# Kernel tuning notes

Hardware: AMD Instinct MI355X
Metric: run time of the kernel (lower is better)

Reference implementation:

```python
import jax, jax.numpy as jnp
import numpy as np

B, C, D, O = 64, 64, 512, 256
N_REG, G = 8, 8  # 8 regions of 8 channels


def setup_inputs() -> dict:
    key = jax.random.key(0)
    ks = jax.random.split(key, 9)
    std = 0.02  # init_weights_classify: normal(0, 0.02) for Linear weights, zero bias
    x = jax.random.normal(ks[0], (B, C, D), dtype=jnp.float32)
    region_indices = jnp.arange(C, dtype=jnp.int32).reshape(N_REG, G)
    # attn_fc: Linear(2D -> D), ReLU, Linear(D -> 1)
    W1 = jax.random.normal(ks[1], (2 * D, D), dtype=jnp.float32) * std
    b1 = jnp.zeros((D,), jnp.float32)
    W2 = jax.random.normal(ks[2], (D, 1), dtype=jnp.float32) * std
    b2 = jnp.zeros((1,), jnp.float32)
    # gcn1: Linear(D -> D); gcn2: Linear(D -> O)
    Wg1 = jax.random.normal(ks[3], (D, D), dtype=jnp.float32) * std
    bg1 = jnp.zeros((D,), jnp.float32)
    Wg2 = jax.random.normal(ks[4], (D, O), dtype=jnp.float32) * std
    bg2 = jnp.zeros((O,), jnp.float32)
    return {"x": x, "W1": W1, "b1": b1, "W2": W2, "b2": b2,
            "Wg1": Wg1, "bg1": bg1, "Wg2": Wg2, "bg2": bg2,
            "region_indices": region_indices}


def _leaky_relu02(z):
    return jnp.where(z >= 0, z, 0.2 * z)


def reference(x, W1, b1, W2, b2, Wg1, bg1, Wg2, bg2, region_indices):
    Bb, Cc, Dd = x.shape
    n_reg, g = region_indices.shape
    # channel -> region id; mask[i,j] = same region and i != j
    rid = jnp.zeros((Cc,), jnp.int32).at[region_indices.reshape(-1)].set(
        jnp.repeat(jnp.arange(n_reg, dtype=jnp.int32), g))
    idx = jnp.arange(Cc)
    mask = (rid[:, None] == rid[None, :]) & (idx[:, None] != idx[None, :])  # [C, C]
    # attn_fc on cat(x_i, x_j): split first linear to avoid [B,C,C,2D] concat
    a = x @ W1[:Dd]   # [B, C, D]
    bpart = x @ W1[Dd:]  # [B, C, D]
    h = jax.nn.relu(a[:, :, None, :] + bpart[:, None, :, :] + b1)  # [B, C, C, D]
    scores = jnp.einsum('bijd,do->bij', h, W2) + b2[0]  # [B, C, C]
    scores = jnp.where(mask[None, :, :], scores, -jnp.inf)
    adj = jax.nn.softmax(scores, axis=-1)  # [B, C, C]
    # gcn1: adj @ x -> Linear -> LeakyReLU(0.2); residual mix
    m1 = jnp.einsum('bij,bjd->bid', adj, x)
    x1 = _leaky_relu02(m1 @ Wg1 + bg1)
    x1 = 0.5 * x1 + 0.5 * x
    # gcn2
    m2 = jnp.einsum('bij,bjd->bid', adj, x1)
    out = _leaky_relu02(m2 @ Wg2 + bg2)  # [B, C, O]
    return out
```

## Files before the change

### kernel.cpp

```cpp
#include <hip/hip_runtime.h>
#include <math.h>

#define B_   64
#define C_   64
#define D_   512
#define O_   256
#define G_   8
#define M_   4096

typedef __attribute__((ext_vector_type(8))) short s16x8;
typedef __attribute__((ext_vector_type(4))) float f32x4;
typedef unsigned short u16;
typedef unsigned int   u32;

__device__ __forceinline__ float bf2f(u16 u) { return __uint_as_float(((u32)u) << 16); }
__device__ __forceinline__ u16 f2bf(float f) {
    u32 u = __float_as_uint(f);
    return (u16)((u + 0x7FFFu + ((u >> 16) & 1u)) >> 16);
}
__device__ __forceinline__ void gload16(const void* g, void* l) {
    __builtin_amdgcn_global_load_lds((const __attribute__((address_space(1))) u32*)g,
                                     (__attribute__((address_space(3))) u32*)l, 16, 0, 0);
}
__device__ __forceinline__ void xcd_swz(int& bx, int& by) {
    int nx = (int)gridDim.x;
    int L = bx + by * nx;
    int nwg = nx * (int)gridDim.y;
    int nid = (L & 7) * (nwg >> 3) + (L >> 3);
    bx = nid & (nx - 1);
    by = nid / nx;
}

__global__ __launch_bounds__(256)
void prep_kernel(const float* __restrict__ x, u16* __restrict__ x_bf,
                 const float* __restrict__ W1, u16* __restrict__ W1t,
                 const float* __restrict__ Wg1, u16* __restrict__ Wg1t,
                 const float* __restrict__ Wg2, u16* __restrict__ Wg2t)
{
    __shared__ float tile[32][33];
    const int bx = blockIdx.x, tid = threadIdx.x;
    if (bx < 1024) {
        size_t i = ((size_t)bx * 256 + tid) * 8;
        const float4* p = (const float4*)(x + i);
        float4 v0 = p[0], v1 = p[1];
        s16x8 o;
        o[0] = (short)f2bf(v0.x); o[1] = (short)f2bf(v0.y);
        o[2] = (short)f2bf(v0.z); o[3] = (short)f2bf(v0.w);
        o[4] = (short)f2bf(v1.x); o[5] = (short)f2bf(v1.y);
        o[6] = (short)f2bf(v1.z); o[7] = (short)f2bf(v1.w);
        *(s16x8*)(x_bf + i) = o;
        return;
    }
    const float* src; u16* dst; int k0, n0, nsrc, obase;
    if (bx < 1536) {
        int idx = bx - 1024, h = idx >> 8, t = idx & 255;
        src = W1 + (size_t)h * 512 * 512; dst = W1t; obase = h * 512;
        k0 = (t >> 4) * 32; n0 = (t & 15) * 32; nsrc = 512;
    } else if (bx < 1792) {
        int t = bx - 1536;
        src = Wg1; dst = Wg1t; obase = 0;
        k0 = (t >> 4) * 32; n0 = (t & 15) * 32; nsrc = 512;
    } else {
        int t = bx - 1792;
        src = Wg2; dst = Wg2t; obase = 0;
        k0 = (t >> 3) * 32; n0 = (t & 7) * 32; nsrc = 256;
    }
    int tx = tid & 31, ty = tid >> 5;
    #pragma unroll
    for (int j = 0; j < 4; j++)
        tile[ty + j * 8][tx] = src[(size_t)(k0 + ty + j * 8) * nsrc + n0 + tx];
    __syncthreads();
    #pragma unroll
    for (int j = 0; j < 4; j++)
        dst[(size_t)(obase + n0 + ty + j * 8) * 512 + k0 + tx] = f2bf(tile[tx][ty + j * 8]);
}

template<int BM, int BN, int EPI>
__global__ __launch_bounds__(256)
void mfma_gemm(const u16* __restrict__ A, const u16* __restrict__ Bt,
               u16* __restrict__ Obf0, u16* __restrict__ Obf1,
               const float* __restrict__ bias, float* __restrict__ Of)
{
    constexpr int K = 512, BK = 64, NT = K / BK;
    constexpr int MR = BM / 32, NR = BN / 32;
    constexpr int CA = BM / 32, CB = BN / 32;

    __shared__ __align__(16) u16 As[2][BM * BK];
    __shared__ __align__(16) u16 Bs[2][BN * BK];

    const int tid = threadIdx.x;
    const int lane = tid & 63;
    const int w = tid >> 6, wr = w >> 1, wc = w & 1;
    const int lr = lane & 15, lq = lane >> 4;
    int bx = blockIdx.x, by = blockIdx.y;
    xcd_swz(bx, by);
    const int m0 = by * BM, n0 = bx * BN;

    const int sr  = tid >> 3;
    const int ss  = tid & 7;
    const int gsl = ss ^ (sr & 7);

    f32x4 acc[MR][NR] = {};

    auto stage = [&](int buf, int kt) {
        #pragma unroll
        for (int ch = 0; ch < CA; ch++)
            gload16(A + (size_t)(m0 + ch * 32 + sr) * K + kt + gsl * 8,
                    &As[buf][ch * 2048 + tid * 8]);
        #pragma unroll
        for (int ch = 0; ch < CB; ch++)
            gload16(Bt + (size_t)(n0 + ch * 32 + sr) * K + kt + gsl * 8,
                    &Bs[buf][ch * 2048 + tid * 8]);
    };

    stage(0, 0);
    int cur = 0;
    for (int t = 0; t < NT; t++) {
        __syncthreads();
        if (t + 1 < NT) stage(cur ^ 1, (t + 1) * BK);
        const u16* as = As[cur]; const u16* bs = Bs[cur];
        #pragma unroll
        for (int ks = 0; ks < 2; ks++) {
            s16x8 af[MR], bfv[NR];
            #pragma unroll
            for (int m = 0; m < MR; m++) {
                int r = wr * (BM / 2) + m * 16 + lr;
                af[m] = *(const s16x8*)(as + r * 64 + (((ks * 4 + lq) ^ (r & 7)) * 8));
            }
            #pragma unroll
            for (int n = 0; n < NR; n++) {
                int r = wc * (BN / 2) + n * 16 + lr;
                bfv[n] = *(const s16x8*)(bs + r * 64 + (((ks * 4 + lq) ^ (r & 7)) * 8));
            }
            #pragma unroll
            for (int m = 0; m < MR; m++)
                #pragma unroll
                for (int n = 0; n < NR; n++)
                    acc[m][n] = __builtin_amdgcn_mfma_f32_16x16x32_bf16(af[m], bfv[n], acc[m][n], 0, 0, 0);
        }
        cur ^= 1;
    }

    #pragma unroll
    for (int m = 0; m < MR; m++) {
        #pragma unroll
        for (int n = 0; n < NR; n++) {
            #pragma unroll
            for (int j = 0; j < 4; j++) {
                int row = m0 + wr * (BM / 2) + m * 16 + lq * 4 + j;
                int col = n0 + wc * (BN / 2) + n * 16 + lr;
                float v = acc[m][n][j];
                if (EPI == 0) {
                    if (col < 512) Obf0[(size_t)row * 512 + col] = f2bf(v);
                    else           Obf1[(size_t)row * 512 + col - 512] = f2bf(v);
                } else {
                    v += bias[col];
                    v = (v >= 0.f) ? v : 0.2f * v;
                    Of[(size_t)row * 256 + col] = v;
                }
            }
        }
    }
}

__global__ __launch_bounds__(256)
void scores_m1_kernel(const u16* __restrict__ a_bf, const u16* __restrict__ bp_bf,
                      const u16* __restrict__ x_bf,
                      const float* __restrict__ b1, const float* __restrict__ W2,
                      const float* __restrict__ b2,
                      const int* __restrict__ region_indices,
                      float* __restrict__ adjw, u16* __restrict__ m1)
{
    __shared__ __align__(16) u16 bp_lds[64 * 512];
    __shared__ __align__(16) u16 x_lds[64 * 512];
    __shared__ int ri_lds[64];
    __shared__ int rid_lds[64];

    int L = blockIdx.x;
    int nid = ((L & 7) << 5) + (L >> 3);
    const int b = nid >> 2, q = nid & 3;
    const int tid = threadIdx.x, lane = tid & 63, w = tid >> 6;

    #pragma unroll
    for (int it = 0; it < 16; it++) {
        gload16(bp_bf + (size_t)b * 32768 + it * 2048 + tid * 8, bp_lds + it * 2048 + tid * 8);
        gload16(x_bf  + (size_t)b * 32768 + it * 2048 + tid * 8, x_lds  + it * 2048 + tid * 8);
    }
    if (tid < 64) {
        int c = region_indices[tid];
        ri_lds[tid] = c;
        rid_lds[c] = tid >> 3;
    }

    const int d0 = lane * 8;
    float4 b1a = *(const float4*)(b1 + d0), b1b = *(const float4*)(b1 + d0 + 4);
    float4 w2a = *(const float4*)(W2 + d0), w2b = *(const float4*)(W2 + d0 + 4);
    float b1v[8] = { b1a.x, b1a.y, b1a.z, b1a.w, b1b.x, b1b.y, b1b.z, b1b.w };
    float w2v[8] = { w2a.x, w2a.y, w2a.z, w2a.w, w2b.x, w2b.y, w2b.z, w2b.w };
    const float bias2 = b2[0];

    __syncthreads();

    for (int rr = 0; rr < 4; rr++) {
        const int i = q * 16 + w * 4 + rr;
        const int bi = b * 64 + i;
        const int r = rid_lds[i];
        int mem[8];
        #pragma unroll
        for (int m = 0; m < 8; m++) mem[m] = ri_lds[r * 8 + m];

        s16x8 a8 = *(const s16x8*)(a_bf + (size_t)bi * 512 + d0);
        float ai[8];
        #pragma unroll
        for (int t = 0; t < 8; t++) ai[t] = bf2f((u16)a8[t]) + b1v[t];

        float p[8];
        #pragma unroll
        for (int m = 0; m < 8; m++) {
            s16x8 bv = *(const s16x8*)(bp_lds + mem[m] * 512 + d0);
            float s = 0.f;
            #pragma unroll
            for (int t = 0; t < 8; t++) {
                float h = ai[t] + bf2f((u16)bv[t]);
                s += fmaxf(h, 0.f) * w2v[t];
            }
            p[m] = s;
        }
        #pragma unroll
        for (int off = 32; off >= 1; off >>= 1)
            #pragma unroll
            for (int m = 0; m < 8; m++) p[m] += __shfl_xor(p[m], off);

        float scmax = -INFINITY;
        #pragma unroll
        for (int m = 0; m < 8; m++) {
            p[m] = (mem[m] == i) ? -INFINITY : p[m] + bias2;
            scmax = fmaxf(scmax, p[m]);
        }
        float esum = 0.f;
        #pragma unroll
        for (int m = 0; m < 8; m++) {
            p[m] = (mem[m] == i) ? 0.f : __expf(p[m] - scmax);
            esum += p[m];
        }
        const float inv = 1.f / esum;

        float accv[8] = {};
        #pragma unroll
        for (int m = 0; m < 8; m++) {
            p[m] *= inv;
            s16x8 xv = *(const s16x8*)(x_lds + mem[m] * 512 + d0);
            #pragma unroll
            for (int t = 0; t < 8; t++) accv[t] += p[m] * bf2f((u16)xv[t]);
        }
        s16x8 o;
        #pragma unroll
        for (int t = 0; t < 8; t++) o[t] = (short)f2bf(accv[t]);
        *(s16x8*)(m1 + (size_t)bi * 512 + d0) = o;
        if (lane < 8) adjw[(size_t)bi * 8 + lane] = p[lane];
    }
}

__global__ __launch_bounds__(256)
void gemm2_m2_kernel(const u16* __restrict__ A, const u16* __restrict__ Bt,
                     const float* __restrict__ bias, const float* __restrict__ xres,
                     const float* __restrict__ adjw, const int* __restrict__ region_indices,
                     u16* __restrict__ m2)
{
    constexpr int K = 512, BK = 64, NT = K / BK;
    __shared__ __align__(16) u16 As[2][64 * 64];
    __shared__ __align__(16) u16 Bs[2][64 * 64];
    __shared__ __align__(16) u16 x1s[64 * 72];
    __shared__ int ri_lds[64];
    __shared__ int rid_lds[64];

    const int tid = threadIdx.x;
    const int lane = tid & 63;
    const int w = tid >> 6, wr = w >> 1, wc = w & 1;
    const int lr = lane & 15, lq = lane >> 4;
    int bx = blockIdx.x, by = blockIdx.y;
    xcd_swz(bx, by);
    const int b = by, n0 = bx * 64;
    const int m0 = b * 64;

    const int sr = tid >> 3, ss = tid & 7;
    const int gsl = ss ^ (sr & 7);

    if (tid < 64) {
        int c = region_indices[tid];
        ri_lds[tid] = c;
        rid_lds[c] = tid >> 3;
    }

    f32x4 acc[2][2] = {};

    auto stage = [&](int buf, int kt) {
        #pragma unroll
        for (int ch = 0; ch < 2; ch++)
            gload16(A + (size_t)(m0 + ch * 32 + sr) * K + kt + gsl * 8,
                    &As[buf][ch * 2048 + tid * 8]);
        #pragma unroll
        for (int ch = 0; ch < 2; ch++)
            gload16(Bt + (size_t)(n0 + ch * 32 + sr) * K + kt + gsl * 8,
                    &Bs[buf][ch * 2048 + tid * 8]);
    };

    stage(0, 0);
    int cur = 0;
    for (int t = 0; t < NT; t++) {
        __syncthreads();
        if (t + 1 < NT) stage(cur ^ 1, (t + 1) * BK);
        const u16* as = As[cur]; const u16* bs = Bs[cur];
        #pragma unroll
        for (int ks = 0; ks < 2; ks++) {
            s16x8 af[2], bfv[2];
            #pragma unroll
            for (int m = 0; m < 2; m++) {
                int r = wr * 32 + m * 16 + lr;
                af[m] = *(const s16x8*)(as + r * 64 + (((ks * 4 + lq) ^ (r & 7)) * 8));
            }
            #pragma unroll
            for (int n = 0; n < 2; n++) {
                int r = wc * 32 + n * 16 + lr;
                bfv[n] = *(const s16x8*)(bs + r * 64 + (((ks * 4 + lq) ^ (r & 7)) * 8));
            }
            #pragma unroll
            for (int m = 0; m < 2; m++)
                #pragma unroll
                for (int n = 0; n < 2; n++)
                    acc[m][n] = __builtin_amdgcn_mfma_f32_16x16x32_bf16(af[m], bfv[n], acc[m][n], 0, 0, 0);
        }
        cur ^= 1;
    }

    #pragma unroll
    for (int m = 0; m < 2; m++) {
        #pragma unroll
        for (int n = 0; n < 2; n++) {
            #pragma unroll
            for (int j = 0; j < 4; j++) {
                int lrow = wr * 32 + m * 16 + lq * 4 + j;
                int lcol = wc * 32 + n * 16 + lr;
                float v = acc[m][n][j] + bias[n0 + lcol];
                v = (v >= 0.f) ? v : 0.2f * v;
                v = 0.5f * v + 0.5f * xres[(size_t)(m0 + lrow) * 512 + n0 + lcol];
                x1s[lrow * 72 + lcol] = f2bf(v);
            }
        }
    }
    __syncthreads();

    const int i = tid >> 2, cb = tid & 3, c0 = cb * 16;
    const int bi = m0 + i;
    const int r = rid_lds[i];
    float acc2[16] = {};
    #pragma unroll
    for (int m = 0; m < 8; m++) {
        float wm = adjw[(size_t)bi * 8 + m];
        int j = ri_lds[r * 8 + m];
        #pragma unroll
        for (int cc = 0; cc < 2; cc++) {
            s16x8 v = *(const s16x8*)(x1s + j * 72 + c0 + cc * 8);
            #pragma unroll
            for (int t = 0; t < 8; t++) acc2[cc * 8 + t] += wm * bf2f((u16)v[t]);
        }
    }
    #pragma unroll
    for (int cc = 0; cc < 2; cc++) {
        s16x8 o;
        #pragma unroll
        for (int t = 0; t < 8; t++) o[t] = (short)f2bf(acc2[cc * 8 + t]);
        *(s16x8*)(m2 + (size_t)bi * 512 + n0 + c0 + cc * 8) = o;
    }
}

extern "C" void kernel_launch(void* const* d_in, const int* in_sizes, int n_in,
                              void* d_out, int out_size, void* d_ws, size_t ws_size,
                              hipStream_t stream) {
    const float* x    = (const float*)d_in[0];
    const float* W1   = (const float*)d_in[1];
    const float* b1   = (const float*)d_in[2];
    const float* W2   = (const float*)d_in[3];
    const float* b2   = (const float*)d_in[4];
    const float* Wg1  = (const float*)d_in[5];
    const float* bg1  = (const float*)d_in[6];
    const float* Wg2  = (const float*)d_in[7];
    const float* bg2  = (const float*)d_in[8];
    const int* region_indices = (const int*)d_in[9];
    float* out = (float*)d_out;

    char* ws = (char*)d_ws;
    const size_t MB = 1024 * 1024;
    u16*   x_bf  = (u16*)(ws);
    u16*   W1t   = (u16*)(ws + 4 * MB);
    u16*   Wg1t  = (u16*)(ws + 5 * MB);
    u16*   Wg2t  = (u16*)(ws + 5 * MB + 512 * 1024);
    u16*   a_bf  = (u16*)(ws + 6 * MB);
    u16*   bp_bf = (u16*)(ws + 10 * MB);
    u16*   m1_bf = (u16*)(ws + 14 * MB);
    u16*   m2_bf = (u16*)(ws + 18 * MB);
    float* adjw  = (float*)(ws + 22 * MB);

    prep_kernel<<<1920, 256, 0, stream>>>(x, x_bf, W1, W1t, Wg1, Wg1t, Wg2, Wg2t);

    mfma_gemm<128, 64, 0><<<dim3(16, 32), 256, 0, stream>>>(
        x_bf, W1t, a_bf, bp_bf, nullptr, nullptr);

    scores_m1_kernel<<<256, 256, 0, stream>>>(a_bf, bp_bf, x_bf, b1, W2, b2,
                                              region_indices, adjw, m1_bf);

    gemm2_m2_kernel<<<dim3(8, 64), 256, 0, stream>>>(
        m1_bf, Wg1t, bg1, x, adjw, region_indices, m2_bf);

    mfma_gemm<64, 64, 2><<<dim3(4, 64), 256, 0, stream>>>(
        m2_bf, Wg2t, nullptr, nullptr, bg2, out);
}
```

Before: 120.3 us.

## Enlarge GEMM tiles to 512-thread blocks and read x directly in scores kernel

The first projection GEMM moves from 128x64 tiles with 256 threads to 128x128 tiles with 512 threads, and the gemm2+m2 fused kernel goes from 64-wide to 128-wide N tiles with 512 threads. Each block now covers more output per load of A and B. The scores kernel no longer stages x into LDS and instead reads x rows straight from global memory (likely cache-resident), which halves its LDS footprint and may raise occupancy. The generic GEMM template is split into specialised kernels. The trade-off is fewer blocks on the grid (256 for gemm1, 256 for gemm2) and uncached-in-LDS gathers.

```diff
diff --git a/kernel.cpp b/kernel.cpp
--- a/kernel.cpp
+++ b/kernel.cpp
@@ -75,42 +75,38 @@
         dst[(size_t)(obase + n0 + ty + j * 8) * 512 + k0 + tx] = f2bf(tile[tx][ty + j * 8]);
 }
 
-template<int BM, int BN, int EPI>
-__global__ __launch_bounds__(256)
-void mfma_gemm(const u16* __restrict__ A, const u16* __restrict__ Bt,
-               u16* __restrict__ Obf0, u16* __restrict__ Obf1,
-               const float* __restrict__ bias, float* __restrict__ Of)
+__global__ __launch_bounds__(512)
+void gemm1_kernel(const u16* __restrict__ A, const u16* __restrict__ Bt,
+                  u16* __restrict__ Obf0, u16* __restrict__ Obf1)
 {
     constexpr int K = 512, BK = 64, NT = K / BK;
-    constexpr int MR = BM / 32, NR = BN / 32;
-    constexpr int CA = BM / 32, CB = BN / 32;
-
-    __shared__ __align__(16) u16 As[2][BM * BK];
-    __shared__ __align__(16) u16 Bs[2][BN * BK];
+    __shared__ __align__(16) u16 As[2][128 * 64];
+    __shared__ __align__(16) u16 Bs[2][128 * 64];
 
     const int tid = threadIdx.x;
     const int lane = tid & 63;
-    const int w = tid >> 6, wr = w >> 1, wc = w & 1;
+    const int w = tid >> 6;
+    const int wr = w >> 1, wc = w & 1;
     const int lr = lane & 15, lq = lane >> 4;
     int bx = blockIdx.x, by = blockIdx.y;
     xcd_swz(bx, by);
-    const int m0 = by * BM, n0 = bx * BN;
-
-    const int sr  = tid >> 3;
-    const int ss  = tid & 7;
+    const int m0 = by * 128, n0 = bx * 128;
+
+    const int sr = tid >> 3;
+    const int ss = tid & 7;
     const int gsl = ss ^ (sr & 7);
 
-    f32x4 acc[MR][NR] = {};
+    f32x4 acc[2][4] = {};
 
     auto stage = [&](int buf, int kt) {
         #pragma unroll
-        for (int ch = 0; ch < CA; ch++)
-            gload16(A + (size_t)(m0 + ch * 32 + sr) * K + kt + gsl * 8,
-                    &As[buf][ch * 2048 + tid * 8]);
-        #pragma unroll
-        for (int ch = 0; ch < CB; ch++)
-            gload16(Bt + (size_t)(n0 + ch * 32 + sr) * K + kt + gsl * 8,
-                    &Bs[buf][ch * 2048 + tid * 8]);
+        for (int ch = 0; ch < 2; ch++)
+            gload16(A + (size_t)(m0 + ch * 64 + sr) * K + kt + gsl * 8,
+                    &As[buf][ch * 4096 + tid * 8]);
+        #pragma unroll
+        for (int ch = 0; ch < 2; ch++)
+            gload16(Bt + (size_t)(n0 + ch * 64 + sr) * K + kt + gsl * 8,
+                    &Bs[buf][ch * 4096 + tid * 8]);
     };
 
     stage(0, 0);
@@ -121,43 +117,37 @@
         const u16* as = As[cur]; const u16* bs = Bs[cur];
         #pragma unroll
         for (int ks = 0; ks < 2; ks++) {
-            s16x8 af[MR], bfv[NR];
-            #pragma unroll
-            for (int m = 0; m < MR; m++) {
-                int r = wr * (BM / 2) + m * 16 + lr;
+            s16x8 af[2], bfv[4];
+            #pragma unroll
+            for (int m = 0; m < 2; m++) {
+                int r = wr * 32 + m * 16 + lr;
                 af[m] = *(const s16x8*)(as + r * 64 + (((ks * 4 + lq) ^ (r & 7)) * 8));
             }
             #pragma unroll
-            for (int n = 0; n < NR; n++) {
-                int r = wc * (BN / 2) + n * 16 + lr;
+            for (int n = 0; n < 4; n++) {
+                int r = wc * 64 + n * 16 + lr;
                 bfv[n] = *(const s16x8*)(bs + r * 64 + (((ks * 4 + lq) ^ (r & 7)) * 8));
             }
             #pragma unroll
-            for (int m = 0; m < MR; m++)
+            for (int m = 0; m < 2; m++)
                 #pragma unroll
-                for (int n = 0; n < NR; n++)
+                for (int n = 0; n < 4; n++)
                     acc[m][n] = __builtin_amdgcn_mfma_f32_16x16x32_bf16(af[m], bfv[n], acc[m][n], 0, 0, 0);
         }
         cur ^= 1;
     }
 
     #pragma unroll
-    for (int m = 0; m < MR; m++) {
-        #pragma unroll
-        for (int n = 0; n < NR; n++) {
+    for (int m = 0; m < 2; m++) {
+        #pragma unroll
+        for (int n = 0; n < 4; n++) {
             #pragma unroll
             for (int j = 0; j < 4; j++) {
-                int row = m0 + wr * (BM / 2) + m * 16 + lq * 4 + j;
-                int col = n0 + wc * (BN / 2) + n * 16 + lr;
+                int row = m0 + wr * 32 + m * 16 + lq * 4 + j;
+                int col = n0 + wc * 64 + n * 16 + lr;
                 float v = acc[m][n][j];
-                if (EPI == 0) {
-                    if (col < 512) Obf0[(size_t)row * 512 + col] = f2bf(v);
-                    else           Obf1[(size_t)row * 512 + col - 512] = f2bf(v);
-                } else {
-                    v += bias[col];
-                    v = (v >= 0.f) ? v : 0.2f * v;
-                    Of[(size_t)row * 256 + col] = v;
-                }
+                if (col < 512) Obf0[(size_t)row * 512 + col] = f2bf(v);
+                else           Obf1[(size_t)row * 512 + col - 512] = f2bf(v);
             }
         }
     }
@@ -172,7 +162,6 @@
                       float* __restrict__ adjw, u16* __restrict__ m1)
 {
     __shared__ __align__(16) u16 bp_lds[64 * 512];
-    __shared__ __align__(16) u16 x_lds[64 * 512];
     __shared__ int ri_lds[64];
     __shared__ int rid_lds[64];
 
@@ -182,10 +171,8 @@
     const int tid = threadIdx.x, lane = tid & 63, w = tid >> 6;
 
     #pragma unroll
-    for (int it = 0; it < 16; it++) {
+    for (int it = 0; it < 16; it++)
         gload16(bp_bf + (size_t)b * 32768 + it * 2048 + tid * 8, bp_lds + it * 2048 + tid * 8);
-        gload16(x_bf  + (size_t)b * 32768 + it * 2048 + tid * 8, x_lds  + it * 2048 + tid * 8);
-    }
     if (tid < 64) {
         int c = region_indices[tid];
         ri_lds[tid] = c;
@@ -249,7 +236,7 @@
         #pragma unroll
         for (int m = 0; m < 8; m++) {
             p[m] *= inv;
-            s16x8 xv = *(const s16x8*)(x_lds + mem[m] * 512 + d0);
+            s16x8 xv = *(const s16x8*)(x_bf + ((size_t)(b * 64 + mem[m])) * 512 + d0);
             #pragma unroll
             for (int t = 0; t < 8; t++) accv[t] += p[m] * bf2f((u16)xv[t]);
         }
@@ -261,7 +248,7 @@
     }
 }
 
-__global__ __launch_bounds__(256)
+__global__ __launch_bounds__(512)
 void gemm2_m2_kernel(const u16* __restrict__ A, const u16* __restrict__ Bt,
                      const float* __restrict__ bias, const float* __restrict__ xres,
                      const float* __restrict__ adjw, const int* __restrict__ region_indices,
@@ -269,10 +256,115 @@
 {
     constexpr int K = 512, BK = 64, NT = K / BK;
     __shared__ __align__(16) u16 As[2][64 * 64];
-    __shared__ __align__(16) u16 Bs[2][64 * 64];
-    __shared__ __align__(16) u16 x1s[64 * 72];
+    __shared__ __align__(16) u16 Bs[2][128 * 64];
+    __shared__ __align__(16) u16 x1s[64 * 136];
     __shared__ int ri_lds[64];
     __shared__ int rid_lds[64];
+
+    const int tid = threadIdx.x;
+    const int lane = tid & 63;
+    const int w = tid >> 6;
+    const int wr = w >> 2, wc = w & 3;
+    const int lr = lane & 15, lq = lane >> 4;
+    int bx = blockIdx.x, by = blockIdx.y;
+    xcd_swz(bx, by);
+    const int b = by, n0 = bx * 128, m0 = b * 64;
+
+    const int sr = tid >> 3, ss = tid & 7;
+    const int gsl = ss ^ (sr & 7);
+
+    if (tid < 64) {
+        int c = region_indices[tid];
+        ri_lds[tid] = c;
+        rid_lds[c] = tid >> 3;
+    }
+
+    f32x4 acc[2][2] = {};
+
+    auto stage = [&](int buf, int kt) {
+        gload16(A + (size_t)(m0 + sr) * K + kt + gsl * 8, &As[buf][tid * 8]);
+        #pragma unroll
+        for (int ch = 0; ch < 2; ch++)
+            gload16(Bt + (size_t)(n0 + ch * 64 + sr) * K + kt + gsl * 8,
+                    &Bs[buf][ch * 4096 + tid * 8]);
+    };
+
+    stage(0, 0);
+    int cur = 0;
+    for (int t = 0; t < NT; t++) {
+        __syncthreads();
+        if (t + 1 < NT) stage(cur ^ 1, (t + 1) * BK);
+        const u16* as = As[cur]; const u16* bs = Bs[cur];
+        #pragma unroll
+        for (int ks = 0; ks < 2; ks++) {
+            s16x8 af[2], bfv[2];
+            #pragma unroll
+            for (int m = 0; m < 2; m++) {
+                int r = wr * 32 + m * 16 + lr;
+                af[m] = *(const s16x8*)(as + r * 64 + (((ks * 4 + lq) ^ (r & 7)) * 8));
+            }
+            #pragma unroll
+            for (int n = 0; n < 2; n++) {
+                int r = wc * 32 + n * 16 + lr;
+                bfv[n] = *(const s16x8*)(bs + r * 64 + (((ks * 4 + lq) ^ (r & 7)) * 8));
+            }
+            #pragma unroll
+            for (int m = 0; m < 2; m++)
+                #pragma unroll
+                for (int n = 0; n < 2; n++)
+                    acc[m][n] = __builtin_amdgcn_mfma_f32_16x16x32_bf16(af[m], bfv[n], acc[m][n], 0, 0, 0);
+        }
+        cur ^= 1;
+    }
+
+    #pragma unroll
+    for (int m = 0; m < 2; m++) {
+        #pragma unroll
+        for (int n = 0; n < 2; n++) {
+            #pragma unroll
+            for (int j = 0; j < 4; j++) {
+                int lrow = wr * 32 + m * 16 + lq * 4 + j;
+                int lcol = wc * 32 + n * 16 + lr;
+                float v = acc[m][n][j] + bias[n0 + lcol];
+                v = (v >= 0.f) ? v : 0.2f * v;
+                v = 0.5f * v + 0.5f * xres[(size_t)(m0 + lrow) * 512 + n0 + lcol];
+                x1s[lrow * 136 + lcol] = f2bf(v);
+            }
+        }
+    }
+    __syncthreads();
+
+    const int i = tid >> 3, cb = tid & 7, c0 = cb * 16;
+    const int bi = m0 + i;
+    const int r = rid_lds[i];
+    float acc2[16] = {};
+    #pragma unroll
+    for (int m = 0; m < 8; m++) {
+        float wm = adjw[(size_t)bi * 8 + m];
+        int j = ri_lds[r * 8 + m];
+        #pragma unroll
+        for (int cc = 0; cc < 2; cc++) {
+            s16x8 v = *(const s16x8*)(x1s + j * 136 + c0 + cc * 8);
+            #pragma unroll
+            for (int t = 0; t < 8; t++) acc2[cc * 8 + t] += wm * bf2f((u16)v[t]);
+        }
+    }
+    #pragma unroll
+    for (int cc = 0; cc < 2; cc++) {
+        s16x8 o;
+        #pragma unroll
+        for (int t = 0; t < 8; t++) o[t] = (short)f2bf(acc2[cc * 8 + t]);
+        *(s16x8*)(m2 + (size_t)bi * 512 + n0 + c0 + cc * 8) = o;
+    }
+}
+
+__global__ __launch_bounds__(256)
+void gemm3_kernel(const u16* __restrict__ A, const u16* __restrict__ Bt,
+                  const float* __restrict__ bias, float* __restrict__ Of)
+{
+    constexpr int K = 512, BK = 64, NT = K / BK;
+    __shared__ __align__(16) u16 As[2][64 * 64];
+    __shared__ __align__(16) u16 Bs[2][64 * 64];
 
     const int tid = threadIdx.x;
     const int lane = tid & 63;
@@ -280,17 +372,10 @@
     const int lr = lane & 15, lq = lane >> 4;
     int bx = blockIdx.x, by = blockIdx.y;
     xcd_swz(bx, by);
-    const int b = by, n0 = bx * 64;
-    const int m0 = b * 64;
+    const int m0 = by * 64, n0 = bx * 64;
 
     const int sr = tid >> 3, ss = tid & 7;
     const int gsl = ss ^ (sr & 7);
-
-    if (tid < 64) {
-        int c = region_indices[tid];
-        ri_lds[tid] = c;
-        rid_lds[c] = tid >> 3;
-    }
 
     f32x4 acc[2][2] = {};
 
@@ -339,38 +424,13 @@
         for (int n = 0; n < 2; n++) {
             #pragma unroll
             for (int j = 0; j < 4; j++) {
-                int lrow = wr * 32 + m * 16 + lq * 4 + j;
-                int lcol = wc * 32 + n * 16 + lr;
-                float v = acc[m][n][j] + bias[n0 + lcol];
+                int row = m0 + wr * 32 + m * 16 + lq * 4 + j;
+                int col = n0 + wc * 32 + n * 16 + lr;
+                float v = acc[m][n][j] + bias[col];
                 v = (v >= 0.f) ? v : 0.2f * v;
-                v = 0.5f * v + 0.5f * xres[(size_t)(m0 + lrow) * 512 + n0 + lcol];
-                x1s[lrow * 72 + lcol] = f2bf(v);
-            }
-        }
-    }
-    __syncthreads();
-
-    const int i = tid >> 2, cb = tid & 3, c0 = cb * 16;
-    const int bi = m0 + i;
-    const int r = rid_lds[i];
-    float acc2[16] = {};
-    #pragma unroll
-    for (int m = 0; m < 8; m++) {
-        float wm = adjw[(size_t)bi * 8 + m];
-        int j = ri_lds[r * 8 + m];
-        #pragma unroll
-        for (int cc = 0; cc < 2; cc++) {
-            s16x8 v = *(const s16x8*)(x1s + j * 72 + c0 + cc * 8);
-            #pragma unroll
-            for (int t = 0; t < 8; t++) acc2[cc * 8 + t] += wm * bf2f((u16)v[t]);
-        }
-    }
-    #pragma unroll
-    for (int cc = 0; cc < 2; cc++) {
-        s16x8 o;
-        #pragma unroll
-        for (int t = 0; t < 8; t++) o[t] = (short)f2bf(acc2[cc * 8 + t]);
-        *(s16x8*)(m2 + (size_t)bi * 512 + n0 + c0 + cc * 8) = o;
+                Of[(size_t)row * 256 + col] = v;
+            }
+        }
     }
 }
 
@@ -403,15 +463,13 @@
 
     prep_kernel<<<1920, 256, 0, stream>>>(x, x_bf, W1, W1t, Wg1, Wg1t, Wg2, Wg2t);
 
-    mfma_gemm<128, 64, 0><<<dim3(16, 32), 256, 0, stream>>>(
-        x_bf, W1t, a_bf, bp_bf, nullptr, nullptr);
+    gemm1_kernel<<<dim3(8, 32), 512, 0, stream>>>(x_bf, W1t, a_bf, bp_bf);
 
     scores_m1_kernel<<<256, 256, 0, stream>>>(a_bf, bp_bf, x_bf, b1, W2, b2,
                                               region_indices, adjw, m1_bf);
 
-    gemm2_m2_kernel<<<dim3(8, 64), 256, 0, stream>>>(
+    gemm2_m2_kernel<<<dim3(4, 64), 512, 0, stream>>>(
         m1_bf, Wg1t, bg1, x, adjw, region_indices, m2_bf);
 
-    mfma_gemm<64, 64, 2><<<dim3(4, 64), 256, 0, stream>>>(
-        m2_bf, Wg2t, nullptr, nullptr, bg2, out);
-}
+    gemm3_kernel<<<dim3(4, 64), 256, 0, stream>>>(m2_bf, Wg2t, bg2, out);
+}
```

New measurement: 119.2 us. No clear change (-0.9%).
